# Kernel optimization log

Measured on AMD Instinct MI355X. Metric: run time of the kernel, lower is better.

## Reference

```python
import jax, jax.numpy as jnp
import numpy as np


def setup_inputs() -> dict:
    key = jax.random.key(0)
    k1, k2, k3 = jax.random.split(key, 3)
    B, CIN, T, K = 64, 64, 1, 4096
    COUT, F = 64, 4
    L = F * K  # 16384; gather index space per (b, o)
    x = jax.random.normal(k1, (B, CIN, T, K), dtype=jnp.float32)
    upsample_params = jax.random.normal(k2, (CIN, COUT, F), dtype=jnp.float32)
    indices = jax.random.randint(k3, (L,), 0, L, dtype=jnp.int64 if jax.config.jax_enable_x64 else jnp.int32)
    return {"x": x, "upsample_params": upsample_params, "indices": indices}


def reference(x, upsample_params, indices):
    # x: [B, Cin, T, K]; params: [Cin, Cout, 4] -> res: [B, Cout, 4, K]
    res = jnp.einsum('bitk,iof->bofk', x, upsample_params)
    B, O = res.shape[0], res.shape[1]
    L = indices.shape[0]  # == 4*K
    # torch: flatten + index_select with per-(b,o) offset == gather along last axis
    flat = res.reshape(B, O, L)
    out = jnp.take(flat, indices, axis=2)
    return out.reshape(B, O, 1, L)
```

## Files before the change

### kernel.cpp

```cpp
#include <hip/hip_runtime.h>


typedef __attribute__((ext_vector_type(8))) short short8;
typedef __attribute__((ext_vector_type(4))) float floatx4;

#define NB    64
#define CIN   64
#define COUT  64
#define KDIM  4096
#define LDIM  16384
#define LT    16

__device__ __forceinline__ unsigned short f2bf(float f) {
  union { float f; unsigned u; } v; v.f = f;
  unsigned r = v.u + 0x7FFFu + ((v.u >> 16) & 1u);
  return (unsigned short)(r >> 16);
}

union V16 { uint4 u; short8 s; };

__global__ __launch_bounds__(256) void transpose_bf16(const float* __restrict__ x,
                                                      unsigned short* __restrict__ xt) {
  __shared__ float tile[64 * 65];
  const int t = threadIdx.x;
  const int b = blockIdx.y;
  const int k0 = blockIdx.x * 64;
  const float4* x4 = (const float4*)x;
#pragma unroll
  for (int p = 0; p < 4; ++p) {
    int i  = p * 16 + (t >> 4);
    int kq = t & 15;
    float4 v = x4[(size_t)(b * CIN + i) * (KDIM / 4) + (k0 >> 2) + kq];
    tile[i * 65 + kq * 4 + 0] = v.x;
    tile[i * 65 + kq * 4 + 1] = v.y;
    tile[i * 65 + kq * 4 + 2] = v.z;
    tile[i * 65 + kq * 4 + 3] = v.w;
  }
  __syncthreads();
  unsigned int* xt32 = (unsigned int*)xt;
  const int ip = (t & 31) * 2;
#pragma unroll
  for (int p = 0; p < 8; ++p) {
    int k = p * 8 + (t >> 5);
    unsigned lo = f2bf(tile[ip * 65 + k]);
    unsigned hi = f2bf(tile[(ip + 1) * 65 + k]);
    xt32[((size_t)b * KDIM + k0 + k) * (CIN / 2) + (ip >> 1)] = lo | (hi << 16);
  }
}

__global__ __launch_bounds__(256) void prep_params(const float* __restrict__ params,
                                                   unsigned short* __restrict__ pbf) {
  const int e = blockIdx.x * 256 + threadIdx.x;
  const int f = e >> 12, o = (e >> 6) & 63, i = e & 63;
  pbf[e] = f2bf(params[(i * COUT + o) * 4 + f]);
}

__global__ __launch_bounds__(256) void gemm_gather(const unsigned short* __restrict__ xt,
                                                   const unsigned short* __restrict__ pbf,
                                                   const int* __restrict__ idx,
                                                   float* __restrict__ out) {
  const int t = threadIdx.x;
  const int b = blockIdx.y;
  const int w = t >> 6;
  const int lane = t & 63;
  const int quad = lane >> 4;
  const int lane15 = lane & 15;
  const int o = w * 16 + lane15;

  short8 afrag[4][2];
#pragma unroll
  for (int f = 0; f < 4; ++f)
#pragma unroll
    for (int kt = 0; kt < 2; ++kt) {
      V16 v; v.u = *(const uint4*)(pbf + ((f * COUT + o) * CIN + kt * 32 + quad * 8));
      afrag[f][kt] = v.s;
    }

  const int lbase = blockIdx.x * (LT * 16);
  const unsigned short* xb = xt + (size_t)b * KDIM * CIN;
  const floatx4 zero = {0.f, 0.f, 0.f, 0.f};

  int iv_cur = idx[lbase + lane15];
  int iv_nxt = idx[lbase + 16 + lane15];
  uint4 b0c, b1c;
  {
    const uint4* row = (const uint4*)(xb + (size_t)(iv_cur & (KDIM - 1)) * CIN);
    b0c = row[quad];
    b1c = row[4 + quad];
  }

  for (int it = 0; it < LT; ++it) {
    uint4 b0n = b0c, b1n = b1c;
    int iv_nn = iv_nxt;
    if (it + 1 < LT) {
      const uint4* row = (const uint4*)(xb + (size_t)(iv_nxt & (KDIM - 1)) * CIN);
      b0n = row[quad];
      b1n = row[4 + quad];
      int ln = lbase + (it + 2) * 16 + lane15;
      iv_nn = idx[ln < LDIM ? ln : LDIM - 1];
    }

    V16 v0, v1; v0.u = b0c; v1.u = b1c;
    floatx4 acc[4];
#pragma unroll
    for (int f = 0; f < 4; ++f) {
      acc[f] = __builtin_amdgcn_mfma_f32_16x16x32_bf16(afrag[f][0], v0.s, zero, 0, 0, 0);
      acc[f] = __builtin_amdgcn_mfma_f32_16x16x32_bf16(afrag[f][1], v1.s, acc[f], 0, 0, 0);
    }

    const int fp = iv_cur >> 12;
    const int l = lbase + it * 16 + lane15;
#pragma unroll
    for (int r = 0; r < 4; ++r) {
      float v01 = (fp == 0) ? acc[0][r] : acc[1][r];
      float v23 = (fp == 2) ? acc[2][r] : acc[3][r];
      float v = (fp < 2) ? v01 : v23;
      const int oo = w * 16 + quad * 4 + r;
      out[((size_t)(b * COUT + oo)) * LDIM + l] = v;
    }

    iv_cur = iv_nxt; iv_nxt = iv_nn;
    b0c = b0n; b1c = b1n;
  }
}

extern "C" void kernel_launch(void* const* d_in, const int* in_sizes, int n_in,
                              void* d_out, int out_size, void* d_ws, size_t ws_size,
                              hipStream_t stream) {
  const float* x      = (const float*)d_in[0];
  const float* params = (const float*)d_in[1];
  const int*   idx    = (const int*)d_in[2];
  float* out = (float*)d_out;

  unsigned short* xt  = (unsigned short*)d_ws;
  unsigned short* pbf = (unsigned short*)((char*)d_ws + (64u << 20));

  transpose_bf16<<<dim3(KDIM / 64, NB), 256, 0, stream>>>(x, xt);
  prep_params<<<dim3(64), 256, 0, stream>>>(params, pbf);
  gemm_gather<<<dim3(LDIM / (LT * 16), NB), 256, 0, stream>>>(xt, pbf, idx, out);
}
```

Before: 374.0 us.

## Stage gathered rows into LDS via async global_load_lds with double buffering

```diff
diff --git a/kernel.cpp b/kernel.cpp
--- a/kernel.cpp
+++ b/kernel.cpp
@@ -9,7 +9,7 @@
 #define COUT  64
 #define KDIM  4096
 #define LDIM  16384
-#define LT    16
+#define TILES 8
 
 __device__ __forceinline__ unsigned short f2bf(float f) {
   union { float f; unsigned u; } v; v.f = f;
@@ -18,6 +18,12 @@
 }
 
 union V16 { uint4 u; short8 s; };
+
+__device__ __forceinline__ void gl2lds16(const void* g, void* l) {
+  __builtin_amdgcn_global_load_lds(
+      (const __attribute__((address_space(1))) unsigned int*)g,
+      (__attribute__((address_space(3))) unsigned int*)l, 16, 0, 0);
+}
 
 __global__ __launch_bounds__(256) void transpose_bf16(const float* __restrict__ x,
                                                       unsigned short* __restrict__ xt) {
@@ -59,6 +65,7 @@
                                                    const unsigned short* __restrict__ pbf,
                                                    const int* __restrict__ idx,
                                                    float* __restrict__ out) {
+  __shared__ __align__(16) unsigned short lds[2 * 64 * 64];
   const int t = threadIdx.x;
   const int b = blockIdx.y;
   const int w = t >> 6;
@@ -76,52 +83,63 @@
       afrag[f][kt] = v.s;
     }
 
-  const int lbase = blockIdx.x * (LT * 16);
+  const int lbase = blockIdx.x * (TILES * 64);
   const unsigned short* xb = xt + (size_t)b * KDIM * CIN;
   const floatx4 zero = {0.f, 0.f, 0.f, 0.f};
 
-  int iv_cur = idx[lbase + lane15];
-  int iv_nxt = idx[lbase + 16 + lane15];
-  uint4 b0c, b1c;
-  {
-    const uint4* row = (const uint4*)(xb + (size_t)(iv_cur & (KDIM - 1)) * CIN);
-    b0c = row[quad];
-    b1c = row[4 + quad];
+  const int subrow = lane >> 3;
+  const int chunk  = lane & 7;
+  const int swsrc  = chunk ^ (subrow & 7);
+
+#define STAGE(IT, BS, IVN)                                                          \
+  {                                                                                 \
+    _Pragma("unroll")                                                               \
+    for (int j = 0; j < 2; ++j) {                                                   \
+      int row = w * 16 + j * 8 + subrow;                                            \
+      int iv = __shfl((IVN), row, 64);                                              \
+      const char* src = (const char*)xb + (size_t)(iv & (KDIM - 1)) * 128 + (swsrc << 4); \
+      gl2lds16(src, (void*)&lds[(BS) * 4096 + (w * 16 + j * 8) * 64]);              \
+    }                                                                               \
   }
 
-  for (int it = 0; it < LT; ++it) {
-    uint4 b0n = b0c, b1n = b1c;
-    int iv_nn = iv_nxt;
-    if (it + 1 < LT) {
-      const uint4* row = (const uint4*)(xb + (size_t)(iv_nxt & (KDIM - 1)) * CIN);
-      b0n = row[quad];
-      b1n = row[4 + quad];
-      int ln = lbase + (it + 2) * 16 + lane15;
-      iv_nn = idx[ln < LDIM ? ln : LDIM - 1];
+  int ivv = idx[lbase + lane];
+  int ivn = idx[lbase + 64 + lane];
+  STAGE(0, 0, ivv);
+
+  for (int it = 0; it < TILES; ++it) {
+    __syncthreads();
+    int iv2 = ivn;
+    if (it + 2 < TILES) iv2 = idx[lbase + (it + 2) * 64 + lane];
+    if (it + 1 < TILES) STAGE(it + 1, (it + 1) & 1, ivn);
+
+    const unsigned short* B = &lds[(it & 1) * 4096];
+#pragma unroll
+    for (int nt = 0; nt < 4; ++nt) {
+      const int row = nt * 16 + lane15;
+      const int sw = lane15 & 7;
+      V16 v0, v1;
+      v0.u = *(const uint4*)&B[row * 64 + ((quad ^ sw) << 3)];
+      v1.u = *(const uint4*)&B[row * 64 + (((4 + quad) ^ sw) << 3)];
+      floatx4 acc[4];
+#pragma unroll
+      for (int f = 0; f < 4; ++f) {
+        acc[f] = __builtin_amdgcn_mfma_f32_16x16x32_bf16(afrag[f][0], v0.s, zero, 0, 0, 0);
+        acc[f] = __builtin_amdgcn_mfma_f32_16x16x32_bf16(afrag[f][1], v1.s, acc[f], 0, 0, 0);
+      }
+      const int fsel = __shfl(ivv, nt * 16 + lane15, 64) >> 12;
+      const int l = lbase + it * 64 + nt * 16 + lane15;
+#pragma unroll
+      for (int r = 0; r < 4; ++r) {
+        float v01 = (fsel == 0) ? acc[0][r] : acc[1][r];
+        float v23 = (fsel == 2) ? acc[2][r] : acc[3][r];
+        float v = (fsel < 2) ? v01 : v23;
+        out[((size_t)(b * COUT + w * 16 + quad * 4 + r)) * LDIM + l] = v;
+      }
     }
-
-    V16 v0, v1; v0.u = b0c; v1.u = b1c;
-    floatx4 acc[4];
-#pragma unroll
-    for (int f = 0; f < 4; ++f) {
-      acc[f] = __builtin_amdgcn_mfma_f32_16x16x32_bf16(afrag[f][0], v0.s, zero, 0, 0, 0);
-      acc[f] = __builtin_amdgcn_mfma_f32_16x16x32_bf16(afrag[f][1], v1.s, acc[f], 0, 0, 0);
-    }
-
-    const int fp = iv_cur >> 12;
-    const int l = lbase + it * 16 + lane15;
-#pragma unroll
-    for (int r = 0; r < 4; ++r) {
-      float v01 = (fp == 0) ? acc[0][r] : acc[1][r];
-      float v23 = (fp == 2) ? acc[2][r] : acc[3][r];
-      float v = (fp < 2) ? v01 : v23;
-      const int oo = w * 16 + quad * 4 + r;
-      out[((size_t)(b * COUT + oo)) * LDIM + l] = v;
-    }
-
-    iv_cur = iv_nxt; iv_nxt = iv_nn;
-    b0c = b0n; b1c = b1n;
+    ivv = ivn;
+    ivn = iv2;
   }
+#undef STAGE
 }
 
 extern "C" void kernel_launch(void* const* d_in, const int* in_sizes, int n_in,
@@ -137,5 +155,5 @@
 
   transpose_bf16<<<dim3(KDIM / 64, NB), 256, 0, stream>>>(x, xt);
   prep_params<<<dim3(64), 256, 0, stream>>>(params, pbf);
-  gemm_gather<<<dim3(LDIM / (LT * 16), NB), 256, 0, stream>>>(xt, pbf, idx, out);
+  gemm_gather<<<dim3(LDIM / (TILES * 64), NB), 256, 0, stream>>>(xt, pbf, idx, out);
 }
```

Result: faster. 357.4 us (-4.4%).
